# Kernel tuning notes

Hardware: AMD Instinct MI355X
Metric: run time of the kernel (lower is better)

Reference implementation:

```python
import jax, jax.numpy as jnp
import numpy as np


def _rope(x, C):
    # x: [B, H, W, C]; 2 spatial channel dims -> k_max = C // 4
    B, H, W, _ = x.shape
    k_max = C // 4
    theta = 1.0 / (10000.0 ** (jnp.arange(k_max, dtype=x.dtype) / k_max))
    hh, ww = jnp.meshgrid(jnp.arange(H, dtype=x.dtype), jnp.arange(W, dtype=x.dtype), indexing='ij')
    angles = jnp.concatenate([hh[..., None] * theta, ww[..., None] * theta], axis=-1)  # [H, W, C//2]
    cos, sin = jnp.cos(angles), jnp.sin(angles)
    xr = x.reshape(B, H, W, C // 2, 2)
    x_re, x_im = xr[..., 0], xr[..., 1]
    out = jnp.stack([x_re * cos - x_im * sin, x_im * cos + x_re * sin], axis=-1)
    return out.reshape(B, H, W, C)


def _forward(x, W_qk, b_qk, scale_p, dwc_w, dwc_b, img_H, img_W):
    B, N, C = x.shape
    head_dim = dwc_w.shape[0]
    h = C // head_dim
    f = 3  # focusing_factor

    qk = x @ W_qk.T + b_qk                        # [B, N, 2C]
    q, k = qk[..., :C], qk[..., C:]
    v = x

    q = _rope(q.reshape(B, img_H, img_W, C), C).reshape(B, N, C)
    k = _rope(k.reshape(B, img_H, img_W, C), C).reshape(B, N, C)

    q = jax.nn.elu(q) + 1.0
    k = jax.nn.elu(k) + 1.0

    scale = jax.nn.softplus(scale_p)              # [1, 1, C]
    q = q / scale
    k = k / scale

    q_norm = jnp.linalg.norm(q, axis=-1, keepdims=True)
    k_norm = jnp.linalg.norm(k, axis=-1, keepdims=True)
    q = q ** f
    k = k ** f
    q = q / jnp.linalg.norm(q, axis=-1, keepdims=True) * q_norm
    k = k / jnp.linalg.norm(k, axis=-1, keepdims=True) * k_norm

    q = q.reshape(B, N, h, head_dim).transpose(0, 2, 1, 3)   # [B, h, N, d]
    k = k.reshape(B, N, h, head_dim).transpose(0, 2, 1, 3)
    v = v.reshape(B, N, h, head_dim).transpose(0, 2, 1, 3)

    k_mean = k.mean(axis=2, keepdims=True)                    # [B, h, 1, d]
    z = 1.0 / (jnp.einsum('bhnd,bhmd->bhnm', q, k_mean) + 1e-6)  # [B, h, N, 1]

    s = float(N) ** (-0.5)
    kv = jnp.einsum('bhnd,bhne->bhde', k * s, v * s)          # [B, h, d, d]
    out = jnp.einsum('bhnd,bhde->bhne', q, kv) * z            # [B, h, N, d]
    out = out.transpose(0, 2, 1, 3).reshape(B, N, C)

    # depthwise conv residual on v
    v_img = v.reshape(B * h, img_H, img_W, head_dim).transpose(0, 3, 1, 2)  # [B*h, d, H, W]
    conv = jax.lax.conv_general_dilated(
        v_img, dwc_w, window_strides=(1, 1), padding='SAME',
        dimension_numbers=('NCHW', 'OIHW', 'NCHW'),
        feature_group_count=head_dim) + dwc_b[None, :, None, None]
    out = out + conv.reshape(B, C, N).transpose(0, 2, 1)
    return out


def setup_inputs() -> dict:
    key = jax.random.key(0)
    ks = jax.random.split(key, 6)
    B, img_H, img_W, C, head_dim, ksz = 8, 64, 64, 512, 32, 5
    N = img_H * img_W
    x = jax.random.normal(ks[0], (B, N, C), dtype=jnp.float32)
    W_qk = jax.random.normal(ks[1], (2 * C, C), dtype=jnp.float32) * 0.02
    b_qk = jnp.zeros((2 * C,), dtype=jnp.float32)
    scale_p = jax.random.normal(ks[2], (1, 1, C), dtype=jnp.float32) * 0.02
    fan_out = ksz * ksz  # depthwise: out_channels/groups = 1
    dwc_w = jax.random.normal(ks[3], (head_dim, 1, ksz, ksz), dtype=jnp.float32) * np.sqrt(2.0 / fan_out)
    dwc_b = jnp.zeros((head_dim,), dtype=jnp.float32)
    return {"x": x, "W_qk": W_qk, "b_qk": b_qk, "scale_p": scale_p,
            "dwc_w": dwc_w, "dwc_b": dwc_b, "img_H": img_H, "img_W": img_W}


def reference(x, W_qk, b_qk, scale_p, dwc_w, dwc_b, img_H, img_W):
    return _forward(x, W_qk, b_qk, scale_p, dwc_w, dwc_b, img_H, img_W)
```

## Files before the change

### kernel.cpp

```cpp
#include <hip/hip_runtime.h>
#include <math.h>

#define B_SZ 8
#define IMG_H 64
#define IMG_W 64
#define N_TOK 4096
#define C_DIM 512
#define HEADS 16
#define HDIM 32
#define M_ROWS (B_SZ * N_TOK)
#define QK_COLS (2 * C_DIM)

#define THETA_COEF (-0.07195578415606394f)

typedef __attribute__((ext_vector_type(8))) __bf16 bf16x8;
typedef __attribute__((ext_vector_type(4))) float f32x4;

__device__ __forceinline__ void async_ld16(void* lds, const void* g) {
    __builtin_amdgcn_global_load_lds(
        (const __attribute__((address_space(1))) unsigned*)g,
        (__attribute__((address_space(3))) unsigned*)lds, 16, 0, 0);
}

__device__ __forceinline__ unsigned short f2bf(float f) {
    unsigned u = __float_as_uint(f);
    u += 0x7FFF + ((u >> 16) & 1);
    return (unsigned short)(u >> 16);
}

__global__ __launch_bounds__(256) void prep_kernel(
    const float* __restrict__ x, const float* __restrict__ Wqk,
    const float* __restrict__ scale_p,
    unsigned short* __restrict__ xb, unsigned short* __restrict__ Wb,
    float* __restrict__ lut)
{
    int bid = blockIdx.x;
    int t = threadIdx.x;
    if (bid < 16384) {
        int i = bid * 256 + t;
        float4 v = ((const float4*)x)[i];
        ushort4 o;
        o.x = f2bf(v.x); o.y = f2bf(v.y); o.z = f2bf(v.z); o.w = f2bf(v.w);
        ((ushort4*)xb)[i] = o;
    } else if (bid < 16896) {
        int i = (bid - 16384) * 256 + t;
        float4 v = ((const float4*)Wqk)[i];
        ushort4 o;
        o.x = f2bf(v.x); o.y = f2bf(v.y); o.z = f2bf(v.z); o.w = f2bf(v.w);
        ((ushort4*)Wb)[i] = o;
    } else {
        int idx = (bid - 16896) * 256 + t;
        int pos = idx >> 7, tt = idx & 127;
        float theta = expf((float)tt * THETA_COEF);
        float ang = (float)pos * theta;
        lut[idx] = cosf(ang);
        lut[idx + 8192] = sinf(ang);
        if (idx < 512) lut[16384 + idx] = 1.0f / log1pf(expf(scale_p[idx]));
    }
}

#define GBM 128
#define GBN 128
#define GBK 32

#define EPI_I(I, ACC) do {                                                    \
    float cr = cI, sr = sI;                                                   \
    _Pragma("unroll")                                                         \
    for (int r = 0; r < 4; ++r) {                                             \
        int m = m0 + wm + (I) * 16 + quad * 4 + r;                            \
        float val = (ACC)[r] + bias;                                          \
        float oth = __shfl_xor(val, 1);                                       \
        float rot = is_im ? (val * cr + oth * sr) : (val * cr - oth * sr);    \
        rot = (rot > 0.f) ? (rot + 1.f) : __expf(rot);                        \
        dst[(size_t)m * C_DIM + ch] = rot * rspv;                             \
        float tc = cr * c1 - sr * s1, ts = sr * c1 + cr * s1;                 \
        cr = tc; sr = ts;                                                     \
    }                                                                         \
    float uc = cI * c16 - sI * s16, us = sI * c16 + cI * s16;                 \
    cI = uc; sI = us;                                                         \
} while (0)

#define EPI_J(J, A0, A1, A2, A3) do {                                         \
    int c = n0 + wn + (J) * 16 + l16;                                         \
    int ch = c & 511;                                                         \
    float bias = bqk[c];                                                      \
    float rspv = rsp[ch];                                                     \
    int tt = ch >> 1;                                                         \
    int tl = tt & 127;                                                        \
    float cI, sI, c1, s1, c16, s16;                                           \
    if (tt < 128) {               \
        int pos = ((m0 + wm) & (N_TOK - 1)) >> 6;                             \
        cI = lut[pos * 128 + tl]; sI = lut[pos * 128 + tl + 8192];            \
        c1 = 1.f; s1 = 0.f; c16 = 1.f; s16 = 0.f;                             \
    } else {                  \
        int pos0 = quad * 4;                                                  \
        cI = lut[pos0 * 128 + tl]; sI = lut[pos0 * 128 + tl + 8192];          \
        c1  = lut[128 + tl];       s1  = lut[128 + tl + 8192];                \
        c16 = lut[2048 + tl];      s16 = lut[2048 + tl + 8192];               \
    }                                                                         \
    float* dst = (c < C_DIM) ? qW : kW;                                       \
    EPI_I(0, A0); EPI_I(1, A1); EPI_I(2, A2); EPI_I(3, A3);                   \
} while (0)

__global__ __launch_bounds__(256, 1) void gemm_mfma_kernel(
    const unsigned short* __restrict__ xb,
    const unsigned short* __restrict__ Wb,
    const float* __restrict__ bqk,
    const float* __restrict__ lut,
    float* __restrict__ qW,
    float* __restrict__ kW)
{
    __shared__ char lds[32768];

    const float* rsp = lut + 16384;

    const int t = threadIdx.x;
    const int wave = t >> 6;
    const int lane = t & 63;
    const int quad = lane >> 4;
    const int l16 = lane & 15;
    const int is_im = l16 & 1;

    const int flat = blockIdx.x + 8 * blockIdx.y;
    const int xcd = flat & 7;
    const int ii_ = flat >> 3;
    const int n0 = (ii_ & 7) * GBN;
    const int m0 = (xcd * 32 + (ii_ >> 3)) * GBM;

    const int wm = (wave >> 1) * 64;
    const int wn = (wave & 1) * 64;

    const int srow = t >> 2;
    const int sj = t & 3;

    f32x4 acc00 = {0.f,0.f,0.f,0.f}, acc01 = {0.f,0.f,0.f,0.f},
          acc02 = {0.f,0.f,0.f,0.f}, acc03 = {0.f,0.f,0.f,0.f},
          acc10 = {0.f,0.f,0.f,0.f}, acc11 = {0.f,0.f,0.f,0.f},
          acc12 = {0.f,0.f,0.f,0.f}, acc13 = {0.f,0.f,0.f,0.f},
          acc20 = {0.f,0.f,0.f,0.f}, acc21 = {0.f,0.f,0.f,0.f},
          acc22 = {0.f,0.f,0.f,0.f}, acc23 = {0.f,0.f,0.f,0.f},
          acc30 = {0.f,0.f,0.f,0.f}, acc31 = {0.f,0.f,0.f,0.f},
          acc32 = {0.f,0.f,0.f,0.f}, acc33 = {0.f,0.f,0.f,0.f};

    const int swz = (l16 >> 1) & 3;
    const int co = (quad ^ swz) * 16;

    auto stage = [&](int k0, int b) {
#pragma unroll
        for (int p = 0; p < 2; ++p) {
            int m = p * 64 + srow;
            int jp = sj ^ ((m >> 1) & 3);
            const unsigned short* ga = xb + (size_t)(m0 + m) * C_DIM + k0 + jp * 8;
            async_ld16(lds + b * 16384 + p * 4096 + wave * 1024, ga);
            const unsigned short* gb = Wb + (size_t)(n0 + m) * C_DIM + k0 + jp * 8;
            async_ld16(lds + b * 16384 + 8192 + p * 4096 + wave * 1024, gb);
        }
    };

    stage(0, 0);
    __syncthreads();
    int buf = 0;

    for (int k0 = 0; k0 < C_DIM; k0 += GBK) {
        if (k0 + GBK < C_DIM) stage(k0 + GBK, buf ^ 1);

        const char* As = lds + buf * 16384;
        const char* Bs = As + 8192;
        bf16x8 a0 = *(const bf16x8*)(As + (wm + 0 * 16 + l16) * 64 + co);
        bf16x8 a1 = *(const bf16x8*)(As + (wm + 1 * 16 + l16) * 64 + co);
        bf16x8 a2 = *(const bf16x8*)(As + (wm + 2 * 16 + l16) * 64 + co);
        bf16x8 a3 = *(const bf16x8*)(As + (wm + 3 * 16 + l16) * 64 + co);
        bf16x8 b0 = *(const bf16x8*)(Bs + (wn + 0 * 16 + l16) * 64 + co);
        bf16x8 b1 = *(const bf16x8*)(Bs + (wn + 1 * 16 + l16) * 64 + co);
        bf16x8 b2 = *(const bf16x8*)(Bs + (wn + 2 * 16 + l16) * 64 + co);
        bf16x8 b3 = *(const bf16x8*)(Bs + (wn + 3 * 16 + l16) * 64 + co);

        acc00 = __builtin_amdgcn_mfma_f32_16x16x32_bf16(a0, b0, acc00, 0, 0, 0);
        acc01 = __builtin_amdgcn_mfma_f32_16x16x32_bf16(a0, b1, acc01, 0, 0, 0);
        acc02 = __builtin_amdgcn_mfma_f32_16x16x32_bf16(a0, b2, acc02, 0, 0, 0);
        acc03 = __builtin_amdgcn_mfma_f32_16x16x32_bf16(a0, b3, acc03, 0, 0, 0);
        acc10 = __builtin_amdgcn_mfma_f32_16x16x32_bf16(a1, b0, acc10, 0, 0, 0);
        acc11 = __builtin_amdgcn_mfma_f32_16x16x32_bf16(a1, b1, acc11, 0, 0, 0);
        acc12 = __builtin_amdgcn_mfma_f32_16x16x32_bf16(a1, b2, acc12, 0, 0, 0);
        acc13 = __builtin_amdgcn_mfma_f32_16x16x32_bf16(a1, b3, acc13, 0, 0, 0);
        acc20 = __builtin_amdgcn_mfma_f32_16x16x32_bf16(a2, b0, acc20, 0, 0, 0);
        acc21 = __builtin_amdgcn_mfma_f32_16x16x32_bf16(a2, b1, acc21, 0, 0, 0);
        acc22 = __builtin_amdgcn_mfma_f32_16x16x32_bf16(a2, b2, acc22, 0, 0, 0);
        acc23 = __builtin_amdgcn_mfma_f32_16x16x32_bf16(a2, b3, acc23, 0, 0, 0);
        acc30 = __builtin_amdgcn_mfma_f32_16x16x32_bf16(a3, b0, acc30, 0, 0, 0);
        acc31 = __builtin_amdgcn_mfma_f32_16x16x32_bf16(a3, b1, acc31, 0, 0, 0);
        acc32 = __builtin_amdgcn_mfma_f32_16x16x32_bf16(a3, b2, acc32, 0, 0, 0);
        acc33 = __builtin_amdgcn_mfma_f32_16x16x32_bf16(a3, b3, acc33, 0, 0, 0);

        __syncthreads();
        buf ^= 1;
    }

    EPI_J(0, acc00, acc10, acc20, acc30);
    EPI_J(1, acc01, acc11, acc21, acc31);
    EPI_J(2, acc02, acc12, acc22, acc32);
    EPI_J(3, acc03, acc13, acc23, acc33);
}

__global__ __launch_bounds__(256) void norm_kernel(
    const float* __restrict__ qW, const float* __restrict__ kW,
    float* __restrict__ sq, float* __restrict__ sk)
{
    int wave = threadIdx.x >> 6;
    int lane = threadIdx.x & 63;
    int m = blockIdx.x * 4 + wave;
    const float4* qr = (const float4*)(qW + (size_t)m * C_DIM);
    const float4* kr = (const float4*)(kW + (size_t)m * C_DIM);
    float q2 = 0.f, q6 = 0.f, k2 = 0.f, k6 = 0.f;
#pragma unroll
    for (int l = 0; l < 2; ++l) {
        float4 q4 = qr[lane + l * 64];
        float4 k4 = kr[lane + l * 64];
        float qq;
        qq = q4.x * q4.x; q2 += qq; q6 += qq * qq * qq;
        qq = q4.y * q4.y; q2 += qq; q6 += qq * qq * qq;
        qq = q4.z * q4.z; q2 += qq; q6 += qq * qq * qq;
        qq = q4.w * q4.w; q2 += qq; q6 += qq * qq * qq;
        qq = k4.x * k4.x; k2 += qq; k6 += qq * qq * qq;
        qq = k4.y * k4.y; k2 += qq; k6 += qq * qq * qq;
        qq = k4.z * k4.z; k2 += qq; k6 += qq * qq * qq;
        qq = k4.w * k4.w; k2 += qq; k6 += qq * qq * qq;
    }
#pragma unroll
    for (int off = 32; off > 0; off >>= 1) {
        q2 += __shfl_down(q2, off);
        q6 += __shfl_down(q6, off);
        k2 += __shfl_down(k2, off);
        k6 += __shfl_down(k6, off);
    }
    if (lane == 0) {
        sq[m] = sqrtf(q2) / sqrtf(q6);
        sk[m] = sqrtf(k2) / sqrtf(k6);
    }
}

#define NSPLIT 8
#define ROWS_PER_SPLIT (N_TOK / NSPLIT)

__global__ __launch_bounds__(256) void kv_partial_kernel(
    const float* __restrict__ x, const float* __restrict__ kW,
    const float* __restrict__ sk,
    float* __restrict__ kvp, float* __restrict__ kmp)
{
    int g = blockIdx.x >> 3;
    int split = blockIdx.x & 7;
    int b = g >> 4, h = g & 15;
    int n_start = split * ROWS_PER_SPLIT;

    __shared__ float smem[5120];
    float* kf = smem;
    float* vv = smem + 64 * 36;

    int t = threadIdx.x;
    int wave = t >> 6, lane = t & 63;
    int srow = t >> 3;
    int scol = (t & 7) * 4;
    int d0 = (lane >> 3) * 4;
    int e0 = (lane & 7) * 4;

    float acc[4][4] = {{0.f}};
    float4 kmacc = make_float4(0.f, 0.f, 0.f, 0.f);

    float4 kreg[2], vreg[2];
    float sreg[2];
#pragma unroll
    for (int h2 = 0; h2 < 2; ++h2) {
        int n = n_start + h2 * 32 + srow;
        size_t base = ((size_t)(b * N_TOK + n)) * C_DIM + h * HDIM + scol;
        kreg[h2] = *(const float4*)&kW[base];
        vreg[h2] = *(const float4*)&x[base];
        sreg[h2] = sk[b * N_TOK + n];
    }

    for (int tt = 0; tt < ROWS_PER_SPLIT / 64; ++tt) {
        __syncthreads();
#pragma unroll
        for (int h2 = 0; h2 < 2; ++h2) {
            int row = h2 * 32 + srow;
            float4 k4 = kreg[h2];
            float s = sreg[h2];
            float4 k3;
            k3.x = k4.x * k4.x * k4.x * s;
            k3.y = k4.y * k4.y * k4.y * s;
            k3.z = k4.z * k4.z * k4.z * s;
            k3.w = k4.w * k4.w * k4.w * s;
            *(float4*)&kf[row * 36 + scol] = k3;
            *(float4*)&vv[row * 36 + scol] = vreg[h2];
            kmacc.x += k3.x; kmacc.y += k3.y;
            kmacc.z += k3.z; kmacc.w += k3.w;
        }
        if (tt < ROWS_PER_SPLIT / 64 - 1) {
            int nb = n_start + (tt + 1) * 64;
#pragma unroll
            for (int h2 = 0; h2 < 2; ++h2) {
                int n = nb + h2 * 32 + srow;
                size_t base = ((size_t)(b * N_TOK + n)) * C_DIM + h * HDIM + scol;
                kreg[h2] = *(const float4*)&kW[base];
                vreg[h2] = *(const float4*)&x[base];
                sreg[h2] = sk[b * N_TOK + n];
            }
        }
        __syncthreads();

        const float* kfp = kf + (wave * 16) * 36 + d0;
        const float* vvp = vv + (wave * 16) * 36 + e0;
#pragma unroll
        for (int nn = 0; nn < 16; ++nn) {
            float4 k4 = *(const float4*)(kfp + nn * 36);
            float4 v4 = *(const float4*)(vvp + nn * 36);
            acc[0][0] += k4.x * v4.x; acc[0][1] += k4.x * v4.y;
            acc[0][2] += k4.x * v4.z; acc[0][3] += k4.x * v4.w;
            acc[1][0] += k4.y * v4.x; acc[1][1] += k4.y * v4.y;
            acc[1][2] += k4.y * v4.z; acc[1][3] += k4.y * v4.w;
            acc[2][0] += k4.z * v4.x; acc[2][1] += k4.z * v4.y;
            acc[2][2] += k4.z * v4.z; acc[2][3] += k4.z * v4.w;
            acc[3][0] += k4.w * v4.x; acc[3][1] += k4.w * v4.y;
            acc[3][2] += k4.w * v4.z; acc[3][3] += k4.w * v4.w;
        }
    }

    __syncthreads();
    float* red = smem;
    float* kmr = smem + 4096;
#pragma unroll
    for (int di = 0; di < 4; ++di) {
        float4 v = make_float4(acc[di][0], acc[di][1], acc[di][2], acc[di][3]);
        *(float4*)&red[wave * 1024 + (d0 + di) * 32 + e0] = v;
    }
    *(float4*)&kmr[srow * 32 + scol] = kmacc;
    __syncthreads();

    size_t pbase = (size_t)blockIdx.x * 1024;
    for (int idx = t; idx < 1024; idx += 256) {
        float s = red[idx] + red[1024 + idx] + red[2048 + idx] + red[3072 + idx];
        kvp[pbase + idx] = s;
    }
    if (t < 32) {
        float s = 0.f;
#pragma unroll
        for (int r = 0; r < 32; ++r) s += kmr[r * 32 + t];
        kmp[blockIdx.x * 32 + t] = s;
    }
}

__global__ __launch_bounds__(256) void kv_reduce_kernel(
    const float* __restrict__ kvp, const float* __restrict__ kmp,
    float* __restrict__ kv, float* __restrict__ km)
{
    int g = blockIdx.x;
    int t = threadIdx.x;
    for (int idx = t; idx < 1024; idx += 256) {
        float s = 0.f;
#pragma unroll
        for (int sp = 0; sp < NSPLIT; ++sp)
            s += kvp[((size_t)(g * NSPLIT + sp)) * 1024 + idx];
        int d = idx >> 5, e = idx & 31;
        kv[(size_t)g * 1024 + e * 32 + d] = s * (1.0f / 4096.0f);
    }
    if (t < 32) {
        float s = 0.f;
#pragma unroll
        for (int sp = 0; sp < NSPLIT; ++sp) s += kmp[(g * NSPLIT + sp) * 32 + t];
        km[g * 32 + t] = s * (1.0f / 4096.0f);
    }
}

__global__ __launch_bounds__(256) void attn_out_kernel(
    const float* __restrict__ qW, const float* __restrict__ sq,
    const float* __restrict__ kvT, const float* __restrict__ km,
    float* __restrict__ out)
{
    int g = blockIdx.x;
    int b = g >> 4, h = g & 15;
    int n0 = blockIdx.y * 128;

    __shared__ float qf[16][36];

    int t = threadIdx.x;
    int e = t & 15;
    int nl = t >> 4;
    int sd = e * 2;

    const float* kvg = kvT + (size_t)g * 1024;
    float4 kva[8], kvb[8], kmr[8];
#pragma unroll
    for (int j = 0; j < 8; ++j) {
        kva[j] = *(const float4*)&kvg[e * 32 + j * 4];
        kvb[j] = *(const float4*)&kvg[(e + 16) * 32 + j * 4];
        kmr[j] = *(const float4*)&km[g * 32 + j * 4];
    }

    size_t rbase = ((size_t)(b * N_TOK + n0 + nl)) * C_DIM + h * HDIM;

    float2 q2 = *(const float2*)&qW[rbase + sd];
    float sv = sq[b * N_TOK + n0 + nl];

    for (int ch = 0; ch < 8; ++ch) {
        __syncthreads();
        *(float2*)&qf[nl][sd] =
            make_float2(q2.x * q2.x * q2.x * sv, q2.y * q2.y * q2.y * sv);

        float2 q2n; float svn;
        if (ch < 7) {
            size_t nb = rbase + (size_t)(ch + 1) * 16 * C_DIM;
            q2n = *(const float2*)&qW[nb + sd];
            svn = sq[b * N_TOK + n0 + (ch + 1) * 16 + nl];
        }
        __syncthreads();

        float s1a = 0.f, s1b = 0.f, s2 = 0.f;
#pragma unroll
        for (int j = 0; j < 8; ++j) {
            float4 q4 = *(const float4*)&qf[nl][j * 4];
            s1a += q4.x * kva[j].x + q4.y * kva[j].y
                 + q4.z * kva[j].z + q4.w * kva[j].w;
            s1b += q4.x * kvb[j].x + q4.y * kvb[j].y
                 + q4.z * kvb[j].z + q4.w * kvb[j].w;
            s2  += q4.x * kmr[j].x + q4.y * kmr[j].y
                 + q4.z * kmr[j].z + q4.w * kmr[j].w;
        }
        float z = 1.0f / (s2 + 1e-6f);
        float* op = out + rbase + (size_t)ch * 16 * C_DIM;
        op[e] = s1a * z;
        op[e + 16] = s1b * z;

        if (ch < 7) { q2 = q2n; sv = svn; }
    }
}

__global__ __launch_bounds__(256, 2) void conv_kernel(
    const float* __restrict__ x, const float* __restrict__ w,
    const float* __restrict__ bias, float* __restrict__ out)
{
    __shared__ float wl[25][32];
    int t = threadIdx.x;
    for (int idx = t; idx < 800; idx += 256) {
        int o = idx & 31, tap = idx >> 5;
        wl[tap][o] = w[o * 25 + tap];
    }
    __syncthreads();

    int bi = blockIdx.x >> 3;
    int part = blockIdx.x & 7;
    int b = bi >> 6, i = bi & 63;
    int jg = part * 2 + (t >> 7);
    int cg = t & 127;
    int j0 = jg * 4;
    int o4 = (cg & 7) * 4;

    const float* xbase = x + ((size_t)b * N_TOK) * C_DIM + cg * 4;

    float4 b4 = *(const float4*)&bias[o4];
    float4 acc[4] = {b4, b4, b4, b4};

#pragma unroll
    for (int ki = 0; ki < 5; ++ki) {
        int ii = i + ki - 2;
        if (ii < 0 || ii >= IMG_H) continue;
        const float* xr = xbase + (size_t)ii * 64 * C_DIM;
        float4 row[8];
#pragma unroll
        for (int jx = 0; jx < 8; ++jx) {
            int jj = j0 + jx - 2;
            row[jx] = (jj >= 0 && jj < IMG_W)
                          ? *(const float4*)(xr + (size_t)jj * C_DIM)
                          : make_float4(0.f, 0.f, 0.f, 0.f);
        }
#pragma unroll
        for (int kj = 0; kj < 5; ++kj) {
            float4 w4 = *(const float4*)&wl[ki * 5 + kj][o4];
#pragma unroll
            for (int jo = 0; jo < 4; ++jo) {
                acc[jo].x += w4.x * row[jo + kj].x;
                acc[jo].y += w4.y * row[jo + kj].y;
                acc[jo].z += w4.z * row[jo + kj].z;
                acc[jo].w += w4.w * row[jo + kj].w;
            }
        }
    }

    float* op = out + ((size_t)(b * N_TOK + i * 64 + j0)) * C_DIM + cg * 4;
#pragma unroll
    for (int jo = 0; jo < 4; ++jo) {
        float4 cur = *(float4*)(op + (size_t)jo * C_DIM);
        cur.x += acc[jo].x;
        cur.y += acc[jo].y;
        cur.z += acc[jo].z;
        cur.w += acc[jo].w;
        *(float4*)(op + (size_t)jo * C_DIM) = cur;
    }
}

extern "C" void kernel_launch(void* const* d_in, const int* in_sizes, int n_in,
                              void* d_out, int out_size, void* d_ws, size_t ws_size,
                              hipStream_t stream) {
    const float* x       = (const float*)d_in[0];
    const float* Wqk     = (const float*)d_in[1];
    const float* bqk     = (const float*)d_in[2];
    const float* scale_p = (const float*)d_in[3];
    const float* dwc_w   = (const float*)d_in[4];
    const float* dwc_b   = (const float*)d_in[5];
    float* out = (float*)d_out;
    float* ws = (float*)d_ws;

    float* qW  = ws;
    float* sq  = qW + (size_t)M_ROWS * C_DIM;
    float* sk  = sq + M_ROWS;
    float* kvp = sk + M_ROWS;
    float* kmp = kvp + (size_t)1024 * 1024;
    float* kv  = kmp + 1024 * 32;
    float* km  = kv + 128 * 1024;
    unsigned short* xb = (unsigned short*)(km + 2048);
    unsigned short* Wb = xb + (size_t)M_ROWS * C_DIM;
    float* lut = (float*)(Wb + (size_t)QK_COLS * C_DIM);
    float* kW  = out;

    prep_kernel<<<16928, 256, 0, stream>>>(x, Wqk, scale_p, xb, Wb, lut);

    dim3 gg(QK_COLS / GBN, M_ROWS / GBM);
    gemm_mfma_kernel<<<gg, 256, 0, stream>>>(xb, Wb, bqk, lut, qW, kW);

    norm_kernel<<<M_ROWS / 4, 256, 0, stream>>>(qW, kW, sq, sk);

    kv_partial_kernel<<<128 * NSPLIT, 256, 0, stream>>>(x, kW, sk, kvp, kmp);
    kv_reduce_kernel<<<128, 256, 0, stream>>>(kvp, kmp, kv, km);

    dim3 g4(128, 32);
    attn_out_kernel<<<g4, 256, 0, stream>>>(qW, sq, kv, km, out);

    conv_kernel<<<M_ROWS / 8, 256, 0, stream>>>(x, dwc_w, dwc_b, out);
}
```

Baseline: 340.4 us.

## Fuse attention output and depthwise conv into one kernel via LDS staging

Merges the attention-output kernel and the depthwise conv kernel into a single kernel. Each block keeps its 128x32 attention tile in shared memory, then computes the 5x5 conv for the same head slice and writes out = attn + conv once. This removes one kernel launch and the write-then-read-modify-write round trip of the output tensor through global memory. In exchange it uses more shared memory per block and reads conv halo rows with a narrower per-head access pattern that may coalesce less well.

Measured after the change: 320.5 us. -5.8%, faster.

```diff
diff --git a/kernel.cpp b/kernel.cpp
--- a/kernel.cpp
+++ b/kernel.cpp
@@ -370,18 +370,26 @@
     }
 }
 
-__global__ __launch_bounds__(256) void attn_out_kernel(
+__global__ __launch_bounds__(256) void attn_conv_kernel(
     const float* __restrict__ qW, const float* __restrict__ sq,
     const float* __restrict__ kvT, const float* __restrict__ km,
-    float* __restrict__ out)
+    const float* __restrict__ x, const float* __restrict__ w,
+    const float* __restrict__ wbias, float* __restrict__ out)
 {
     int g = blockIdx.x;
     int b = g >> 4, h = g & 15;
     int n0 = blockIdx.y * 128;
 
     __shared__ float qf[16][36];
+    __shared__ float ob[128][34];
+    __shared__ float wl[25][32];
 
     int t = threadIdx.x;
+    for (int idx = t; idx < 800; idx += 256) {
+        int o = idx & 31, tap = idx >> 5;
+        wl[tap][o] = w[o * 25 + tap];
+    }
+
     int e = t & 15;
     int nl = t >> 4;
     int sd = e * 2;
@@ -425,37 +433,24 @@
                  + q4.z * kmr[j].z + q4.w * kmr[j].w;
         }
         float z = 1.0f / (s2 + 1e-6f);
-        float* op = out + rbase + (size_t)ch * 16 * C_DIM;
-        op[e] = s1a * z;
-        op[e + 16] = s1b * z;
+        ob[ch * 16 + nl][e] = s1a * z;
+        ob[ch * 16 + nl][e + 16] = s1b * z;
 
         if (ch < 7) { q2 = q2n; sv = svn; }
     }
-}
-
-__global__ __launch_bounds__(256, 2) void conv_kernel(
-    const float* __restrict__ x, const float* __restrict__ w,
-    const float* __restrict__ bias, float* __restrict__ out)
-{
-    __shared__ float wl[25][32];
-    int t = threadIdx.x;
-    for (int idx = t; idx < 800; idx += 256) {
-        int o = idx & 31, tap = idx >> 5;
-        wl[tap][o] = w[o * 25 + tap];
-    }
+
     __syncthreads();
 
-    int bi = blockIdx.x >> 3;
-    int part = blockIdx.x & 7;
-    int b = bi >> 6, i = bi & 63;
-    int jg = part * 2 + (t >> 7);
-    int cg = t & 127;
+    int r = t >> 7;
+    int jg = (t >> 3) & 15;
+    int cg = t & 7;
     int j0 = jg * 4;
-    int o4 = (cg & 7) * 4;
-
-    const float* xbase = x + ((size_t)b * N_TOK) * C_DIM + cg * 4;
-
-    float4 b4 = *(const float4*)&bias[o4];
+    int o4 = cg * 4;
+    int i = (n0 >> 6) + r;
+
+    const float* xbase = x + ((size_t)b * N_TOK) * C_DIM + h * HDIM + o4;
+
+    float4 b4 = *(const float4*)&wbias[o4];
     float4 acc[4] = {b4, b4, b4, b4};
 
 #pragma unroll
@@ -484,15 +479,15 @@
         }
     }
 
-    float* op = out + ((size_t)(b * N_TOK + i * 64 + j0)) * C_DIM + cg * 4;
+    float* op = out + ((size_t)(b * N_TOK + i * 64 + j0)) * C_DIM + h * HDIM + o4;
 #pragma unroll
     for (int jo = 0; jo < 4; ++jo) {
-        float4 cur = *(float4*)(op + (size_t)jo * C_DIM);
-        cur.x += acc[jo].x;
-        cur.y += acc[jo].y;
-        cur.z += acc[jo].z;
-        cur.w += acc[jo].w;
-        *(float4*)(op + (size_t)jo * C_DIM) = cur;
+        float4 a = *(const float4*)&ob[r * 64 + j0 + jo][o4];
+        acc[jo].x += a.x;
+        acc[jo].y += a.y;
+        acc[jo].z += a.z;
+        acc[jo].w += a.w;
+        *(float4*)(op + (size_t)jo * C_DIM) = acc[jo];
     }
 }
 
@@ -531,7 +526,5 @@
     kv_reduce_kernel<<<128, 256, 0, stream>>>(kvp, kmp, kv, km);
 
     dim3 g4(128, 32);
-    attn_out_kernel<<<g4, 256, 0, stream>>>(qW, sq, kv, km, out);
-
-    conv_kernel<<<M_ROWS / 8, 256, 0, stream>>>(x, dwc_w, dwc_b, out);
-}
+    attn_conv_kernel<<<g4, 256, 0, stream>>>(qW, sq, kv, km, x, dwc_w, dwc_b, out);
+}
```
